# Kernel optimization log

Hardware: AMD Instinct MI355X
Metric: run time of the kernel (lower is better)

Reference implementation:

```python
import jax, jax.numpy as jnp
import numpy as np

B, T, H, QS = 32, 4096, 512, 512

def setup_inputs() -> dict:
    key = jax.random.key(0)
    k1, k2, k3, k4, k5 = jax.random.split(key, 5)
    query = jax.random.normal(k1, (B, 1, QS), dtype=jnp.float32)
    precomputed_key = jax.random.normal(k2, (B, T, H), dtype=jnp.float32)
    value = jax.random.normal(k3, (B, T, H), dtype=jnp.float32)
    mask = jnp.ones((B, T), dtype=bool)  # unused in original forward
    Wq = jax.random.normal(k4, (H, QS), dtype=jnp.float32) * (1.0 / np.sqrt(QS))
    We = jax.random.normal(k5, (H,), dtype=jnp.float32) * (1.0 / np.sqrt(H))
    return {"query": query, "precomputed_key": precomputed_key, "value": value,
            "mask": mask, "Wq": Wq, "We": We}

def reference(query, precomputed_key, value, mask, Wq, We):
    # query_layer: Linear(query_size -> hidden, no bias): x @ Wq.T
    q = jnp.einsum('bqs,hs->bqh', query, Wq)              # [B,1,H]
    # energy: tanh(q + key) then Linear(hidden -> 1, no bias), squeeze
    scores = jnp.einsum('bth,h->bt', jnp.tanh(q + precomputed_key), We)  # [B,T]
    alphas = jax.nn.softmax(scores, axis=1)               # [B,T]
    # bmm(alphas[B,1,T], value[B,T,D]) -> [B,1,D]
    context = jnp.einsum('bt,btd->bd', alphas, value)[:, None, :]
    return context, alphas
```

## Files before the change

kernel.cpp:

```cpp
#include <hip/hip_runtime.h>
#include <math.h>

#define BB 32
#define TT 4096
#define HH 512
#define QQS 512
#define TS 64
#define CH 64

#define TANH_K 2.8853900817779268f

__device__ inline float fast_exp2(float x) {
#if __has_builtin(__builtin_amdgcn_exp2f)
    return __builtin_amdgcn_exp2f(x);
#else
    return __expf(x * 0.6931471805599453f);
#endif
}
__device__ inline float fast_rcp(float x) {
#if __has_builtin(__builtin_amdgcn_rcpf)
    return __builtin_amdgcn_rcpf(x);
#else
    return 1.f / x;
#endif
}

__device__ inline float wave_reduce_sum(float v) {
#pragma unroll
    for (int off = 32; off > 0; off >>= 1) v += __shfl_xor(v, off, 64);
    return v;
}

__device__ inline float wave_reduce_max(float v) {
#pragma unroll
    for (int off = 32; off > 0; off >>= 1) v = fmaxf(v, __shfl_xor(v, off, 64));
    return v;
}

__global__ void qproj_kernel(const float* __restrict__ query,
                             const float* __restrict__ Wq,
                             float* __restrict__ qout) {
    int wid  = (blockIdx.x * blockDim.x + threadIdx.x) >> 6;
    int lane = threadIdx.x & 63;
    int b = wid >> 9;
    int h = wid & (HH - 1);
    const float4* qr = (const float4*)(query + (size_t)b * QQS);
    const float4* wr = (const float4*)(Wq + (size_t)h * QQS);
    float4 a0 = qr[lane],      w0 = wr[lane];
    float4 a1 = qr[lane + 64], w1 = wr[lane + 64];
    float acc = a0.x * w0.x + a0.y * w0.y + a0.z * w0.z + a0.w * w0.w
              + a1.x * w1.x + a1.y * w1.y + a1.z * w1.z + a1.w * w1.w;
    acc = wave_reduce_sum(acc);
    if (lane == 0) qout[wid] = acc;
}

__device__ inline float tanh_term(float k, float qc, float w, float p) {
    float e = fast_exp2(fmaf(k, TANH_K, qc));
    float r = fast_rcp(e + 1.f);
    float th = fmaf(-2.f, r, 1.f);
    return fmaf(th, w, p);
}

__global__ __launch_bounds__(256) void fused_kernel(
        const float* __restrict__ key, const float* __restrict__ value,
        const float* __restrict__ qb,  const float* __restrict__ We,
        float* __restrict__ alphas, float* __restrict__ mbuf,
        float* __restrict__ zbuf,   float* __restrict__ part) {
    __shared__ float s_lds[CH];
    __shared__ float e_lds[CH];
    __shared__ float ctx_lds[HH];

    int b = blockIdx.x / TS, c = blockIdx.x % TS;
    int tid = threadIdx.x;
    int w = tid >> 6, lane = tid & 63;
    size_t row0 = (size_t)b * TT + (size_t)c * CH;

    const float4* qv = (const float4*)(qb + (size_t)b * HH);
    const float4* wv = (const float4*)We;
    float4 q0 = qv[lane], q1 = qv[lane + 64];
    float4 w0 = wv[lane], w1 = wv[lane + 64];
    q0.x *= TANH_K; q0.y *= TANH_K; q0.z *= TANH_K; q0.w *= TANH_K;
    q1.x *= TANH_K; q1.y *= TANH_K; q1.z *= TANH_K; q1.w *= TANH_K;

#pragma unroll 2
    for (int rr = 0; rr < CH / 8; ++rr) {
        int r0 = rr * 8 + w, r1 = r0 + 4;
        const float4* k0p = (const float4*)(key + (row0 + r0) * HH);
        const float4* k1p = (const float4*)(key + (row0 + r1) * HH);
        float4 ka = k0p[lane], kb = k0p[lane + 64];
        float4 kc = k1p[lane], kd = k1p[lane + 64];
        float p0 = 0.f, p1 = 0.f;
        p0 = tanh_term(ka.x, q0.x, w0.x, p0);
        p0 = tanh_term(ka.y, q0.y, w0.y, p0);
        p0 = tanh_term(ka.z, q0.z, w0.z, p0);
        p0 = tanh_term(ka.w, q0.w, w0.w, p0);
        p0 = tanh_term(kb.x, q1.x, w1.x, p0);
        p0 = tanh_term(kb.y, q1.y, w1.y, p0);
        p0 = tanh_term(kb.z, q1.z, w1.z, p0);
        p0 = tanh_term(kb.w, q1.w, w1.w, p0);
        p1 = tanh_term(kc.x, q0.x, w0.x, p1);
        p1 = tanh_term(kc.y, q0.y, w0.y, p1);
        p1 = tanh_term(kc.z, q0.z, w0.z, p1);
        p1 = tanh_term(kc.w, q0.w, w0.w, p1);
        p1 = tanh_term(kd.x, q1.x, w1.x, p1);
        p1 = tanh_term(kd.y, q1.y, w1.y, p1);
        p1 = tanh_term(kd.z, q1.z, w1.z, p1);
        p1 = tanh_term(kd.w, q1.w, w1.w, p1);
        float a0 = __shfl_xor(p0, 32, 64);
        float a1 = __shfl_xor(p1, 32, 64);
        float ws = (lane < 32) ? (p0 + a0) : (p1 + a1);
#pragma unroll
        for (int off = 16; off > 0; off >>= 1) ws += __shfl_xor(ws, off, 64);
        if ((lane & 31) == 0) s_lds[(lane < 32) ? r0 : r1] = ws;
    }
    __syncthreads();

    if (w == 0) {
        float s = s_lds[lane];
        float m = wave_reduce_max(s);
        float e = __expf(s - m);
        e_lds[lane] = e;
        alphas[row0 + lane] = e;
        float z = wave_reduce_sum(e);
        if (lane == 0) {
            mbuf[b * TS + c] = m;
            zbuf[b * TS + c] = z;
        }
    }
    __syncthreads();

    int d4 = tid & 127, rg = tid >> 7;
    const float4* vp = (const float4*)(value + row0 * HH);
    float4 acc = make_float4(0.f, 0.f, 0.f, 0.f);
#pragma unroll 4
    for (int r = rg * 32; r < rg * 32 + 32; ++r) {
        float a = e_lds[r];
        float4 v = vp[(size_t)r * (HH / 4) + d4];
        acc.x += a * v.x; acc.y += a * v.y; acc.z += a * v.z; acc.w += a * v.w;
    }
    if (rg == 0) ((float4*)ctx_lds)[d4] = acc;
    __syncthreads();
    if (rg == 1) {
        float4 t = ((float4*)ctx_lds)[d4];
        t.x += acc.x; t.y += acc.y; t.z += acc.z; t.w += acc.w;
        ((float4*)(part + ((size_t)c * BB + b) * HH))[d4] = t;
    }
}

__global__ void finalize_kernel(const float* __restrict__ mbuf,
                                const float* __restrict__ zbuf,
                                const float* __restrict__ part,
                                float* __restrict__ alphas,
                                float* __restrict__ ctx) {
    int tid = threadIdx.x, lane = tid & 63;
    __shared__ float scale[TS];
    if (blockIdx.x < BB) {
        int b = blockIdx.x;
        float m_l = mbuf[b * TS + lane];
        float z_l = zbuf[b * TS + lane];
        float M = wave_reduce_max(m_l);
        float Z = wave_reduce_sum(__expf(m_l - M) * z_l);
        float invZ = 1.f / Z;
        if (tid < TS) scale[tid] = __expf(m_l - M) * invZ;
        __syncthreads();
        float4* ap = (float4*)(alphas + (size_t)b * TT);
#pragma unroll
        for (int i = 0; i < 4; ++i) {
            int idx = tid + i * 256;
            float4 a = ap[idx];
            float s = scale[idx >> 4];
            a.x *= s; a.y *= s; a.z *= s; a.w *= s;
            ap[idx] = a;
        }
    } else {
        int i = blockIdx.x - BB;
        int b = i >> 1;
        int d = (i & 1) * 256 + tid;
        float m_l = mbuf[b * TS + lane];
        float z_l = zbuf[b * TS + lane];
        float M = wave_reduce_max(m_l);
        float Z = wave_reduce_sum(__expf(m_l - M) * z_l);
        if (tid < TS) scale[tid] = __expf(m_l - M) / Z;
        __syncthreads();
        float s = 0.f;
#pragma unroll
        for (int c2 = 0; c2 < TS; ++c2)
            s += scale[c2] * part[((size_t)c2 * BB + b) * HH + d];
        ctx[(size_t)b * HH + d] = s;
    }
}

extern "C" void kernel_launch(void* const* d_in, const int* in_sizes, int n_in,
                              void* d_out, int out_size, void* d_ws, size_t ws_size,
                              hipStream_t stream) {
    const float* query = (const float*)d_in[0];
    const float* key   = (const float*)d_in[1];
    const float* value = (const float*)d_in[2];
    const float* Wq    = (const float*)d_in[4];
    const float* We    = (const float*)d_in[5];

    float* ctx    = (float*)d_out;
    float* alphas = (float*)d_out + BB * HH;

    float* qbuf   = (float*)d_ws;
    float* mbuf   = qbuf + BB * HH;
    float* zbuf   = mbuf + BB * TS;
    float* part   = zbuf + BB * TS;

    qproj_kernel<<<(BB * HH) / 4, 256, 0, stream>>>(query, Wq, qbuf);
    fused_kernel<<<BB * TS, 256, 0, stream>>>(key, value, qbuf, We, alphas, mbuf, zbuf, part);
    finalize_kernel<<<BB + 2 * BB, 256, 0, stream>>>(mbuf, zbuf, part, alphas, ctx);
}
```

Before: 109.1 us.

## Load value rows alongside key rows and halve chunk size per block

Each block now handles 32 rows instead of 64, and the grid doubles to 128 chunks per batch. Each wave loads its 8 value rows into registers together with the key rows, so value traffic overlaps the tanh/score computation rather than waiting until after the softmax. The per-chunk max is combined across waves through LDS, the weighted value sum runs in registers, and the finalize kernel now reduces over 128 chunk partials. This raises register pressure and doubles the partial-context buffer and the finalize reduction work.

```diff
diff --git a/kernel.cpp b/kernel.cpp
--- a/kernel.cpp
+++ b/kernel.cpp
@@ -5,16 +5,17 @@
 #define TT 4096
 #define HH 512
 #define QQS 512
-#define TS 64
-#define CH 64
+#define TS 128
+#define CH 32
 
 #define TANH_K 2.8853900817779268f
+#define LOG2E  1.4426950408889634f
 
 __device__ inline float fast_exp2(float x) {
 #if __has_builtin(__builtin_amdgcn_exp2f)
     return __builtin_amdgcn_exp2f(x);
 #else
-    return __expf(x * 0.6931471805599453f);
+    return exp2f(x);
 #endif
 }
 __device__ inline float fast_rcp(float x) {
@@ -28,12 +29,6 @@
 __device__ inline float wave_reduce_sum(float v) {
 #pragma unroll
     for (int off = 32; off > 0; off >>= 1) v += __shfl_xor(v, off, 64);
-    return v;
-}
-
-__device__ inline float wave_reduce_max(float v) {
-#pragma unroll
-    for (int off = 32; off > 0; off >>= 1) v = fmaxf(v, __shfl_xor(v, off, 64));
     return v;
 }
 
@@ -66,13 +61,12 @@
         const float* __restrict__ qb,  const float* __restrict__ We,
         float* __restrict__ alphas, float* __restrict__ mbuf,
         float* __restrict__ zbuf,   float* __restrict__ part) {
+    __shared__ float m_lds[4];
     __shared__ float s_lds[CH];
-    __shared__ float e_lds[CH];
-    __shared__ float ctx_lds[HH];
+    __shared__ float4 ctx_lds[4][HH / 4];
 
     int b = blockIdx.x / TS, c = blockIdx.x % TS;
-    int tid = threadIdx.x;
-    int w = tid >> 6, lane = tid & 63;
+    int tid = threadIdx.x, w = tid >> 6, lane = tid & 63;
     size_t row0 = (size_t)b * TT + (size_t)c * CH;
 
     const float4* qv = (const float4*)(qb + (size_t)b * HH);
@@ -82,68 +76,94 @@
     q0.x *= TANH_K; q0.y *= TANH_K; q0.z *= TANH_K; q0.w *= TANH_K;
     q1.x *= TANH_K; q1.y *= TANH_K; q1.z *= TANH_K; q1.w *= TANH_K;
 
-#pragma unroll 2
-    for (int rr = 0; rr < CH / 8; ++rr) {
-        int r0 = rr * 8 + w, r1 = r0 + 4;
-        const float4* k0p = (const float4*)(key + (row0 + r0) * HH);
-        const float4* k1p = (const float4*)(key + (row0 + r1) * HH);
-        float4 ka = k0p[lane], kb = k0p[lane + 64];
-        float4 kc = k1p[lane], kd = k1p[lane + 64];
-        float p0 = 0.f, p1 = 0.f;
-        p0 = tanh_term(ka.x, q0.x, w0.x, p0);
-        p0 = tanh_term(ka.y, q0.y, w0.y, p0);
-        p0 = tanh_term(ka.z, q0.z, w0.z, p0);
-        p0 = tanh_term(ka.w, q0.w, w0.w, p0);
-        p0 = tanh_term(kb.x, q1.x, w1.x, p0);
-        p0 = tanh_term(kb.y, q1.y, w1.y, p0);
-        p0 = tanh_term(kb.z, q1.z, w1.z, p0);
-        p0 = tanh_term(kb.w, q1.w, w1.w, p0);
-        p1 = tanh_term(kc.x, q0.x, w0.x, p1);
-        p1 = tanh_term(kc.y, q0.y, w0.y, p1);
-        p1 = tanh_term(kc.z, q0.z, w0.z, p1);
-        p1 = tanh_term(kc.w, q0.w, w0.w, p1);
-        p1 = tanh_term(kd.x, q1.x, w1.x, p1);
-        p1 = tanh_term(kd.y, q1.y, w1.y, p1);
-        p1 = tanh_term(kd.z, q1.z, w1.z, p1);
-        p1 = tanh_term(kd.w, q1.w, w1.w, p1);
-        float a0 = __shfl_xor(p0, 32, 64);
-        float a1 = __shfl_xor(p1, 32, 64);
-        float ws = (lane < 32) ? (p0 + a0) : (p1 + a1);
-#pragma unroll
-        for (int off = 16; off > 0; off >>= 1) ws += __shfl_xor(ws, off, 64);
-        if ((lane & 31) == 0) s_lds[(lane < 32) ? r0 : r1] = ws;
-    }
-    __syncthreads();
-
-    if (w == 0) {
-        float s = s_lds[lane];
-        float m = wave_reduce_max(s);
-        float e = __expf(s - m);
-        e_lds[lane] = e;
-        alphas[row0 + lane] = e;
-        float z = wave_reduce_sum(e);
-        if (lane == 0) {
-            mbuf[b * TS + c] = m;
+    const float4* kb4 = (const float4*)(key + row0 * HH);
+    const float4* vb4 = (const float4*)(value + row0 * HH);
+
+    float4 vA0, vB0, vA1, vB1, vA2, vB2, vA3, vB3;
+    float4 vA4, vB4, vA5, vB5, vA6, vB6, vA7, vB7;
+    float s0, s1, s2, s3, s4, s5, s6, s7;
+
+#define ROW(J, VA, VB, SS) { \
+    int r = w + 4 * (J); \
+    const float4* kp = kb4 + (size_t)r * (HH / 4); \
+    const float4* vp = vb4 + (size_t)r * (HH / 4); \
+    VA = vp[lane]; VB = vp[lane + 64]; \
+    float4 ka = kp[lane], kc = kp[lane + 64]; \
+    float p = 0.f; \
+    p = tanh_term(ka.x, q0.x, w0.x, p); \
+    p = tanh_term(ka.y, q0.y, w0.y, p); \
+    p = tanh_term(ka.z, q0.z, w0.z, p); \
+    p = tanh_term(ka.w, q0.w, w0.w, p); \
+    p = tanh_term(kc.x, q1.x, w1.x, p); \
+    p = tanh_term(kc.y, q1.y, w1.y, p); \
+    p = tanh_term(kc.z, q1.z, w1.z, p); \
+    p = tanh_term(kc.w, q1.w, w1.w, p); \
+    _Pragma("unroll") \
+    for (int off = 32; off > 0; off >>= 1) p += __shfl_xor(p, off, 64); \
+    SS = p; \
+    if (lane == 0) s_lds[r] = p; \
+}
+    ROW(0, vA0, vB0, s0)
+    ROW(1, vA1, vB1, s1)
+    ROW(2, vA2, vB2, s2)
+    ROW(3, vA3, vB3, s3)
+    ROW(4, vA4, vB4, s4)
+    ROW(5, vA5, vB5, s5)
+    ROW(6, vA6, vB6, s6)
+    ROW(7, vA7, vB7, s7)
+#undef ROW
+
+    float m_w = fmaxf(fmaxf(fmaxf(s0, s1), fmaxf(s2, s3)),
+                      fmaxf(fmaxf(s4, s5), fmaxf(s6, s7)));
+    if (lane == 0) m_lds[w] = m_w;
+    __syncthreads();
+    float m_c = fmaxf(fmaxf(m_lds[0], m_lds[1]), fmaxf(m_lds[2], m_lds[3]));
+
+    float e0 = fast_exp2((s0 - m_c) * LOG2E);
+    float e1 = fast_exp2((s1 - m_c) * LOG2E);
+    float e2 = fast_exp2((s2 - m_c) * LOG2E);
+    float e3 = fast_exp2((s3 - m_c) * LOG2E);
+    float e4 = fast_exp2((s4 - m_c) * LOG2E);
+    float e5 = fast_exp2((s5 - m_c) * LOG2E);
+    float e6 = fast_exp2((s6 - m_c) * LOG2E);
+    float e7 = fast_exp2((s7 - m_c) * LOG2E);
+
+    float4 accA, accB;
+    accA.x = e0 * vA0.x; accA.y = e0 * vA0.y; accA.z = e0 * vA0.z; accA.w = e0 * vA0.w;
+    accB.x = e0 * vB0.x; accB.y = e0 * vB0.y; accB.z = e0 * vB0.z; accB.w = e0 * vB0.w;
+#define ACC(E, VA, VB) \
+    accA.x = fmaf(E, VA.x, accA.x); accA.y = fmaf(E, VA.y, accA.y); \
+    accA.z = fmaf(E, VA.z, accA.z); accA.w = fmaf(E, VA.w, accA.w); \
+    accB.x = fmaf(E, VB.x, accB.x); accB.y = fmaf(E, VB.y, accB.y); \
+    accB.z = fmaf(E, VB.z, accB.z); accB.w = fmaf(E, VB.w, accB.w);
+    ACC(e1, vA1, vB1) ACC(e2, vA2, vB2) ACC(e3, vA3, vB3)
+    ACC(e4, vA4, vB4) ACC(e5, vA5, vB5) ACC(e6, vA6, vB6) ACC(e7, vA7, vB7)
+#undef ACC
+
+    ctx_lds[w][lane] = accA;
+    ctx_lds[w][lane + 64] = accB;
+    __syncthreads();
+
+    if (tid < 128) {
+        float4 t0 = ctx_lds[0][tid], t1 = ctx_lds[1][tid];
+        float4 t2 = ctx_lds[2][tid], t3 = ctx_lds[3][tid];
+        float4 t;
+        t.x = (t0.x + t1.x) + (t2.x + t3.x);
+        t.y = (t0.y + t1.y) + (t2.y + t3.y);
+        t.z = (t0.z + t1.z) + (t2.z + t3.z);
+        t.w = (t0.w + t1.w) + (t2.w + t3.w);
+        ((float4*)(part + ((size_t)c * BB + b) * HH))[tid] = t;
+    } else if (tid < 160) {
+        int l = tid - 128;
+        float e = fast_exp2((s_lds[l] - m_c) * LOG2E);
+        alphas[row0 + l] = e;
+        float z = e;
+#pragma unroll
+        for (int off = 16; off > 0; off >>= 1) z += __shfl_xor(z, off, 64);
+        if (l == 0) {
+            mbuf[b * TS + c] = m_c;
             zbuf[b * TS + c] = z;
         }
-    }
-    __syncthreads();
-
-    int d4 = tid & 127, rg = tid >> 7;
-    const float4* vp = (const float4*)(value + row0 * HH);
-    float4 acc = make_float4(0.f, 0.f, 0.f, 0.f);
-#pragma unroll 4
-    for (int r = rg * 32; r < rg * 32 + 32; ++r) {
-        float a = e_lds[r];
-        float4 v = vp[(size_t)r * (HH / 4) + d4];
-        acc.x += a * v.x; acc.y += a * v.y; acc.z += a * v.z; acc.w += a * v.w;
-    }
-    if (rg == 0) ((float4*)ctx_lds)[d4] = acc;
-    __syncthreads();
-    if (rg == 1) {
-        float4 t = ((float4*)ctx_lds)[d4];
-        t.x += acc.x; t.y += acc.y; t.z += acc.z; t.w += acc.w;
-        ((float4*)(part + ((size_t)c * BB + b) * HH))[d4] = t;
     }
 }
 
@@ -152,38 +172,42 @@
                                 const float* __restrict__ part,
                                 float* __restrict__ alphas,
                                 float* __restrict__ ctx) {
-    int tid = threadIdx.x, lane = tid & 63;
+    __shared__ float red[8];
     __shared__ float scale[TS];
+    int tid = threadIdx.x, lane = tid & 63, w = tid >> 6;
+    int b = (blockIdx.x < BB) ? blockIdx.x : ((blockIdx.x - BB) >> 1);
+
+    float m_l = -1e30f, z_l = 0.f;
+    if (tid < TS) { m_l = mbuf[b * TS + tid]; z_l = zbuf[b * TS + tid]; }
+    float m = m_l;
+#pragma unroll
+    for (int off = 32; off > 0; off >>= 1) m = fmaxf(m, __shfl_xor(m, off, 64));
+    if (lane == 0) red[w] = m;
+    __syncthreads();
+    float M = fmaxf(fmaxf(red[0], red[1]), fmaxf(red[2], red[3]));
+    float ez = (tid < TS) ? __expf(m_l - M) * z_l : 0.f;
+#pragma unroll
+    for (int off = 32; off > 0; off >>= 1) ez += __shfl_xor(ez, off, 64);
+    if (lane == 0) red[4 + w] = ez;
+    __syncthreads();
+    float Z = (red[4] + red[5]) + (red[6] + red[7]);
+    if (tid < TS) scale[tid] = __expf(m_l - M) / Z;
+    __syncthreads();
+
     if (blockIdx.x < BB) {
-        int b = blockIdx.x;
-        float m_l = mbuf[b * TS + lane];
-        float z_l = zbuf[b * TS + lane];
-        float M = wave_reduce_max(m_l);
-        float Z = wave_reduce_sum(__expf(m_l - M) * z_l);
-        float invZ = 1.f / Z;
-        if (tid < TS) scale[tid] = __expf(m_l - M) * invZ;
-        __syncthreads();
         float4* ap = (float4*)(alphas + (size_t)b * TT);
 #pragma unroll
         for (int i = 0; i < 4; ++i) {
             int idx = tid + i * 256;
             float4 a = ap[idx];
-            float s = scale[idx >> 4];
+            float s = scale[idx >> 3];
             a.x *= s; a.y *= s; a.z *= s; a.w *= s;
             ap[idx] = a;
         }
     } else {
-        int i = blockIdx.x - BB;
-        int b = i >> 1;
-        int d = (i & 1) * 256 + tid;
-        float m_l = mbuf[b * TS + lane];
-        float z_l = zbuf[b * TS + lane];
-        float M = wave_reduce_max(m_l);
-        float Z = wave_reduce_sum(__expf(m_l - M) * z_l);
-        if (tid < TS) scale[tid] = __expf(m_l - M) / Z;
-        __syncthreads();
+        int d = ((blockIdx.x - BB) & 1) * 256 + tid;
         float s = 0.f;
-#pragma unroll
+#pragma unroll 8
         for (int c2 = 0; c2 < TS; ++c2)
             s += scale[c2] * part[((size_t)c2 * BB + b) * HH + d];
         ctx[(size_t)b * HH + d] = s;
```

Measured after the change: 118.3 us. 1.08x slower.
